# Kernel tuning notes

Hardware: AMD Instinct MI355X
Metric: run time of the kernel (lower is better)

## Reference

```python
import jax, jax.numpy as jnp
import numpy as np
from jax import lax

# Per-tensor power-of-two scales (ScalingImplType.CONST / POWER_OF_TWO in Brevitas)
S_ACT8 = 2.0 ** -4   # 8-bit signed input quant scale
S_ACT4 = 2.0 ** -1   # 4-bit signed input quant scale
S_W = 2.0 ** -2      # per-tensor weight quant scale
S_RELU = 2.0 ** -2   # 4-bit unsigned QuantReLU scale


def fq(x, scale, qmin, qmax):
    # fake-quant with straight-through estimator (STE)
    q = jnp.clip(jnp.round(x / scale), qmin, qmax) * scale
    return x + lax.stop_gradient(q - x)


def fq_signed(x, scale, bits):
    return fq(x, scale, -(2 ** (bits - 1)), 2 ** (bits - 1) - 1)


def fq_uint(x, scale, bits):
    return fq(x, scale, 0, 2 ** bits - 1)


def qconv(x, w, in_bits, w_bits, s_in, stride=1, padding=0, groups=1):
    xq = fq_signed(x, s_in, in_bits)
    wq = fq_signed(w, S_W, w_bits)
    return lax.conv_general_dilated(
        xq, wq, (stride, stride), [(padding, padding)] * 2,
        feature_group_count=groups,
        dimension_numbers=('NCHW', 'OIHW', 'NCHW'))


def maxpool(x, k, s):
    return lax.reduce_window(x, -jnp.inf, lax.max,
                             (1, 1, k, k), (1, 1, s, s), 'VALID')


def dwsep(x, dw, pw):
    c = x.shape[1]
    x = qconv(x, dw, 4, 4, S_ACT4, padding=1, groups=c)  # depthwise 3x3
    x = qconv(x, pw, 4, 4, S_ACT4)                       # pointwise 1x1
    return x


def qrelu4(x):
    return fq_uint(jax.nn.relu(x), S_RELU, 4)


def setup_inputs() -> dict:
    key = jax.random.key(0)
    ks = jax.random.split(key, 10)
    B = 1024
    mk = lambda k, shp, sc=0.5: jax.random.normal(k, shp, jnp.float32) * sc
    return {
        'x': jax.random.normal(ks[0], (B, 3, 32, 32), jnp.float32),
        'w0': mk(ks[1], (3, 3, 1, 1)),
        'dw1': mk(ks[2], (3, 1, 3, 3)),
        'pw1': mk(ks[3], (32, 3, 1, 1)),
        'dw2': mk(ks[4], (32, 1, 3, 3)),
        'pw2': mk(ks[5], (64, 32, 1, 1)),
        'dw3': mk(ks[6], (64, 1, 3, 3)),
        'pw3': mk(ks[7], (128, 64, 1, 1)),
        'wc1': mk(ks[8], (256, 128, 1, 1)),
        'wc2': mk(ks[9], (10, 256, 1, 1)),
    }


def reference(x, w0, dw1, pw1, dw2, pw2, dw3, pw3, wc1, wc2):
    # features
    h = qconv(x, w0, 8, 8, S_ACT8)            # 1x1, 3->3, 8-bit
    h = dwsep(h, dw1, pw1)                    # 3->32, 32x32
    h = qrelu4(h)
    h = maxpool(h, 2, 2)                      # 16x16
    h = dwsep(h, dw2, pw2)                    # 32->64
    h = qrelu4(h)
    h = maxpool(h, 2, 2)                      # 8x8
    h = dwsep(h, dw3, pw3)                    # 64->128
    h = qrelu4(h)
    h = maxpool(h, 8, 1)                      # 1x1
    # classifier
    h = qconv(h, wc1, 4, 4, S_ACT4)           # 128->256
    h = qrelu4(h)
    h = qconv(h, wc2, 4, 4, S_ACT4)           # 256->10
    h = fq_signed(h, S_ACT8, 8)               # output quant int8
    return h
```

## Files before the change

kernel.cpp:

```cpp
#include <hip/hip_runtime.h>

typedef int v4i __attribute__((ext_vector_type(4)));

#define W0i   0
#define DW1i  9
#define PW1i  36
#define DW2i  132
#define WC1p  3556
#define WC2p  11748
#define PW2Fb 12388
#define PW3Fb 12900
#define DW2pk 14948
#define DW3pk 15092
#define WTOT  15380

__device__ __attribute__((aligned(16))) int g_wsq[WTOT];

__device__ __forceinline__ int iclamp(int v, int lo, int hi) {
  return v < lo ? lo : (v > hi ? hi : v);
}
__device__ __forceinline__ int rne4(int a) {
  return (a + 1 + ((a >> 2) & 1)) >> 2;
}
__device__ __forceinline__ int rne32(int a) {
  return (a + 15 + ((a >> 5) & 1)) >> 5;
}

__device__ __forceinline__ void bar_lds() {
  asm volatile("s_waitcnt lgkmcnt(0)\n\ts_barrier" ::: "memory");
}

__device__ __forceinline__ int dot4(int a, int b, int c) {
#if defined(__has_builtin) && __has_builtin(__builtin_amdgcn_sdot4)
  return __builtin_amdgcn_sdot4(a, b, c, false);
#else
  c += ((a << 24) >> 24) * ((b << 24) >> 24);
  c += ((a << 16) >> 24) * ((b << 16) >> 24);
  c += ((a <<  8) >> 24) * ((b <<  8) >> 24);
  c += (a >> 24) * (b >> 24);
  return c;
#endif
}

__device__ __forceinline__ int alignb(int hi, int lo, int sh) {
#if defined(__has_builtin) && __has_builtin(__builtin_amdgcn_alignbyte)
  return __builtin_amdgcn_alignbyte(hi, lo, sh);
#else
  return (int)(((((unsigned long long)(unsigned)hi) << 32) |
                (unsigned)lo) >> (8 * sh));
#endif
}

__device__ __forceinline__ int pack3(int a, int b, int c) {
  return (a & 0xff) | ((b & 0xff) << 8) | ((c & 0xff) << 16);
}

__device__ __forceinline__ int pk_mad16(int a, int b, int c) {
  int d;
  asm("v_pk_mad_i16 %0, %1, %2, %3" : "=v"(d) : "v"(a), "v"(b), "v"(c));
  return d;
}
__device__ __forceinline__ int pk_add16(int a, int b) {
  int d;
  asm("v_pk_add_i16 %0, %1, %2" : "=v"(d) : "v"(a), "v"(b));
  return d;
}
__device__ __forceinline__ int pk_ashr16(int sh, int a) {
  int d;
  asm("v_pk_ashrrev_i16 %0, %1, %2" : "=v"(d) : "v"(sh), "v"(a));
  return d;
}
__device__ __forceinline__ int pk_max16(int a, int b) {
  int d;
  asm("v_pk_max_i16 %0, %1, %2" : "=v"(d) : "v"(a), "v"(b));
  return d;
}
__device__ __forceinline__ int pk_min16(int a, int b) {
  int d;
  asm("v_pk_min_i16 %0, %1, %2" : "=v"(d) : "v"(a), "v"(b));
  return d;
}
__device__ __forceinline__ int rne4s_pk(int a) {
  const int sh = 0x00020002, one = 0x00010001;
  int t = pk_ashr16(sh, a);
  t &= one;
  t += one;
  int s4 = pk_add16(a, t);
  int r = pk_ashr16(sh, s4);
  r = pk_max16(r, (int)0xFFF8FFF8);
  r = pk_min16(r, 0x00070007);
  return r;
}

__device__ __forceinline__ int max4(v4i d) {
  int a = d[0] > d[1] ? d[0] : d[1];
  int b = d[2] > d[3] ? d[2] : d[3];
  return a > b ? a : b;
}

__global__ __launch_bounds__(256) void prep_weights(
    const float* __restrict__ w0,  const float* __restrict__ dw1,
    const float* __restrict__ pw1, const float* __restrict__ dw2,
    const float* __restrict__ pw2, const float* __restrict__ dw3,
    const float* __restrict__ pw3, const float* __restrict__ wc1,
    const float* __restrict__ wc2) {
  int t = blockIdx.x * blockDim.x + threadIdx.x;
  if (t >= WTOT) return;
  if (t >= DW2i && t < WC1p) return;
  if (t < DW2i) {
    float w; int lo = -8, hi = 7;
    if (t < DW1i)      { w = w0[t];        lo = -128; hi = 127; }
    else if (t < PW1i)   w = dw1[t - DW1i];
    else                 w = pw1[t - PW1i];
    g_wsq[t] = iclamp((int)rintf(w * 4.f), lo, hi);
  } else if (t < PW2Fb) {
    const float* src = (t < WC2p) ? wc1 + (t - WC1p) * 4
                                  : wc2 + (t - WC2p) * 4;
    int p = 0;
#pragma unroll
    for (int b = 0; b < 4; b++) {
      int c = iclamp((int)rintf(src[b] * 4.f), -8, 7);
      p |= (c & 0xff) << (8 * b);
    }
    g_wsq[t] = p;
  } else if (t < DW2pk) {
    int i = t - PW2Fb;
    int nt = i >> 7, r = i & 127, lane = r >> 1, dw = r & 1;
    int n = nt * 16 + (lane & 15);
    int kb = (lane >> 4) * 8 + dw * 4;
    int p = 0;
#pragma unroll
    for (int b = 0; b < 4; b++) {
      int c = iclamp((int)rintf(pw2[n * 32 + kb + b] * 4.f), -8, 7);
      p |= (c & 0xff) << (8 * b);
    }
    g_wsq[t] = p;
  } else if (t < DW2pk + 144) {
    int i = t - DW2pk;
    int cq = i / 18, r = i - cq * 18, t9 = r >> 1, par = r & 1;
    int wl = iclamp((int)rintf(dw2[(cq * 4 + par) * 9 + t9] * 4.f), -8, 7);
    int wh = iclamp((int)rintf(dw2[(cq * 4 + 2 + par) * 9 + t9] * 4.f), -8, 7);
    g_wsq[t] = (wl & 0xFFFF) | (wh << 16);
  } else {
    int i = t - DW3pk;
    int cq = i / 18, r = i - cq * 18, t9 = r >> 1, par = r & 1;
    int wl = iclamp((int)rintf(dw3[(cq * 4 + par) * 9 + t9] * 4.f), -8, 7);
    int wh = iclamp((int)rintf(dw3[(cq * 4 + 2 + par) * 9 + t9] * 4.f), -8, 7);
    g_wsq[t] = (wl & 0xFFFF) | (wh << 16);
  }
}

__global__ __launch_bounds__(256) void prep_weights_pw3(
    const float* __restrict__ pw3) {
  int t = PW3Fb + blockIdx.x * blockDim.x + threadIdx.x;
  if (t >= DW2pk) return;
  int i = t - PW3Fb;
  int g = i >> 7, r = i & 127, lane = r >> 1, dw = r & 1;
  int nt = g >> 1, kh = g & 1;
  int n = nt * 16 + (lane & 15);
  int kb = kh * 32 + (lane >> 4) * 8 + dw * 4;
  int p = 0;
#pragma unroll
  for (int b = 0; b < 4; b++) {
    int c = iclamp((int)rintf(pw3[n * 64 + kb + b] * 4.f), -8, 7);
    p |= (c & 0xff) << (8 * b);
  }
  g_wsq[t] = p;
}

__global__ __launch_bounds__(256, 4) void fused_net(
    const float* __restrict__ x,
    float* __restrict__ out)
{
  const int img = blockIdx.x;
  const int tid = threadIdx.x;
  const int wv = tid >> 6, lane = tid & 63;
  const int lm = lane & 15, kg = lane >> 4;
  const int* __restrict__ wq = g_wsq;

  __shared__ __align__(16) int bufAi[2560];
  __shared__ __align__(16) int bufBi[2592];

  const int ntp = (wv & 1) * 2;
  const long bw0 = *(const long*)(wq + PW2Fb + (ntp * 64 + lane) * 2);
  const long bw1 = *(const long*)(wq + PW2Fb + ((ntp + 1) * 64 + lane) * 2);
  long b0v[2], b1v[2];
#pragma unroll
  for (int h = 0; h < 2; h++) {
    int nt = wv * 2 + h;
    b0v[h] = *(const long*)(wq + PW3Fb + (nt * 2 + 0) * 128 + lane * 2);
    b1v[h] = *(const long*)(wq + PW3Fb + (nt * 2 + 1) * 128 + lane * 2);
  }

  {
    const float* xim = x + (size_t)img * 3072;
    const int p4 = tid * 4;
    float4 v0 = *(const float4*)(xim + p4);
    float4 v1 = *(const float4*)(xim + 1024 + p4);
    float4 v2 = *(const float4*)(xim + 2048 + p4);
    int w[9];
#pragma unroll
    for (int i = 0; i < 9; i++) w[i] = wq[W0i + i];
#define Q8(v) iclamp((int)rintf((v) * 16.f), -128, 127)
    int a0[4] = {Q8(v0.x), Q8(v0.y), Q8(v0.z), Q8(v0.w)};
    int a1[4] = {Q8(v1.x), Q8(v1.y), Q8(v1.z), Q8(v1.w)};
    int a2[4] = {Q8(v2.x), Q8(v2.y), Q8(v2.z), Q8(v2.w)};
#undef Q8
#pragma unroll
    for (int o = 0; o < 3; o++) {
      int pk = 0;
#pragma unroll
      for (int j = 0; j < 4; j++) {
        int s = a0[j] * w[o * 3] + a1[j] * w[o * 3 + 1] + a2[j] * w[o * 3 + 2];
        pk |= (iclamp(rne32(s), -8, 7) & 0xff) << (8 * j);
      }
      bufAi[o * 256 + tid] = pk;
    }
  }
  bar_lds();

  {
    const int py = tid >> 4, px = tid & 15;
    int wr[3][3], wrh[3][3];
#pragma unroll
    for (int c = 0; c < 3; c++)
#pragma unroll
      for (int ky = 0; ky < 3; ky++) {
        int w = pack3(wq[DW1i + c * 9 + ky * 3],
                      wq[DW1i + c * 9 + ky * 3 + 1],
                      wq[DW1i + c * 9 + ky * 3 + 2]);
        wr[c][ky] = w;
        wrh[c][ky] = w << 8;
      }
    const int s = (px & 1) ? 1 : 3;
    const int D0 = (2 * px - 1) >> 2;
    int V[3][4];
#pragma unroll
    for (int r = 0; r < 4; r++) {
      int rr = 2 * py - 1 + r;
      bool ok = (unsigned)rr < 32u;
#pragma unroll
      for (int c = 0; c < 3; c++) {
        int lo = 0, hi = 0;
        if (ok) {
          const int* ap = bufAi + c * 256 + rr * 8;
          if (px > 0)  lo = ap[D0];
          if (px < 15) hi = ap[D0 + 1];
        }
        V[c][r] = alignb(hi, lo, s);
      }
    }
    int a[4];
#pragma unroll
    for (int dy = 0; dy < 2; dy++) {
      int r01[3];
#pragma unroll
      for (int c = 0; c < 3; c++) {
        int acc0 = 0, acc1 = 0;
#pragma unroll
        for (int ky = 0; ky < 3; ky++) {
          acc0 = dot4(V[c][dy + ky], wr[c][ky], acc0);
          acc1 = dot4(V[c][dy + ky], wrh[c][ky], acc1);
        }
        int p = (int)__builtin_amdgcn_perm((unsigned)acc1, (unsigned)acc0,
                                           0x05040100u);
        r01[c] = rne4s_pk(p);
      }
      unsigned t0 = __builtin_amdgcn_perm((unsigned)r01[1], (unsigned)r01[0],
                                          0x0C0C0400u);
      a[2 * dy] = (int)__builtin_amdgcn_perm((unsigned)r01[2], t0, 0x0C040100u);
      unsigned t1 = __builtin_amdgcn_perm((unsigned)r01[1], (unsigned)r01[0],
                                          0x0C0C0602u);
      a[2 * dy + 1] =
          (int)__builtin_amdgcn_perm((unsigned)r01[2], t1, 0x0C060100u);
    }
#pragma unroll
    for (int it = 0; it < 8; it++) {
      int pk = 0;
#pragma unroll
      for (int j = 0; j < 4; j++) {
        int o = it * 4 + j;
        int wpk = pack3(wq[PW1i + o * 3], wq[PW1i + o * 3 + 1],
                        wq[PW1i + o * 3 + 2]);
        int m0 = dot4(a[0], wpk, 0), m1 = dot4(a[1], wpk, 0);
        int m2 = dot4(a[2], wpk, 0), m3 = dot4(a[3], wpk, 0);
        int mx = max(max(m0, m1), max(m2, m3));
        pk |= iclamp(rne4(mx), 0, 7) << (8 * j);
      }
      bufBi[py * 149 + px * 9 + it] = pk;
    }
  }
  bar_lds();

  {
    const int cq = tid >> 5;
    const int rem = tid & 31;
    const int y = rem >> 1, xh = rem & 1, x0 = xh * 8;
    int we[9], wo[9];
    {
      const int2* wp = (const int2*)(wq + DW2pk + cq * 18);
#pragma unroll
      for (int t9 = 0; t9 < 9; t9++) { int2 v = wp[t9]; we[t9] = v.x; wo[t9] = v.y; }
    }
    int acce[8] = {}, acco[8] = {};
#pragma unroll
    for (int ky = 0; ky < 3; ky++) {
      int yy = y + ky - 1;
      if (yy < 0 || yy > 15) continue;
      int rb = yy * 149 + cq;
      int rd[10];
      rd[0] = (x0 > 0) ? bufBi[rb + (x0 - 1) * 9] : 0;
#pragma unroll
      for (int k = 1; k < 9; k++) rd[k] = bufBi[rb + (x0 - 1 + k) * 9];
      rd[9] = (x0 < 8) ? bufBi[rb + (x0 + 8) * 9] : 0;
      int ee[10], eo[10];
#pragma unroll
      for (int k = 0; k < 10; k++) {
        ee[k] = rd[k] & 0x000F000F;
        eo[k] = (rd[k] >> 8) & 0x000F000F;
      }
#pragma unroll
      for (int j = 0; j < 8; j++)
#pragma unroll
        for (int kx = 0; kx < 3; kx++) {
          acce[j] = pk_mad16(ee[j + kx], we[ky * 3 + kx], acce[j]);
          acco[j] = pk_mad16(eo[j + kx], wo[ky * 3 + kx], acco[j]);
        }
    }
    const int py = y >> 1, dy = y & 1;
#pragma unroll
    for (int j = 0; j < 8; j++) {
      int xx = x0 + j;
      int qp = py * 8 + (xx >> 1);
      int q = qp ^ (py & 3);
      int m = q * 4 + dy * 2 + (xx & 1);
      int re = rne4s_pk(acce[j]);
      int ro = rne4s_pk(acco[j]);
      bufAi[m * 10 + cq] = (re & 0x00FF00FF) | ((ro & 0x00FF00FF) << 8);
    }
  }
  bar_lds();

  {
    const int mtb = (wv >> 1) * 8;
    const signed char* Ab = (const signed char*)bufAi;
    signed char* A2c = (signed char*)bufBi;
    const int n0 = ntp * 16 + lm, n1 = (ntp + 1) * 16 + lm;
#pragma unroll 4
    for (int mt = mtb; mt < mtb + 8; mt++) {
      int m = mt * 16 + lm;
      long av = *(const long*)(Ab + m * 40 + kg * 8);
      v4i d0 = __builtin_amdgcn_mfma_i32_16x16x32_i8(av, bw0, (v4i){0, 0, 0, 0},
                                                     0, 0, 0);
      v4i d1 = __builtin_amdgcn_mfma_i32_16x16x32_i8(av, bw1, (v4i){0, 0, 0, 0},
                                                     0, 0, 0);
      int q = mt * 4 + kg;
      int qp = q ^ ((q >> 3) & 3);
      int py = qp >> 3, px = qp & 7;
      int bb = (py * 137 + px * 17) * 4;
      A2c[bb + n0] = (signed char)iclamp(rne4(max4(d0)), 0, 7);
      A2c[bb + n1] = (signed char)iclamp(rne4(max4(d1)), 0, 7);
    }
  }
  bar_lds();

  {
    int cq2 = tid >> 4;
    int s = tid & 15;
    int y = s >> 1, x0 = (s & 1) << 2;
    int we[9], wo[9];
    {
      const int2* wp = (const int2*)(wq + DW3pk + cq2 * 18);
#pragma unroll
      for (int t9 = 0; t9 < 9; t9++) { int2 v = wp[t9]; we[t9] = v.x; wo[t9] = v.y; }
    }
    int acce[4] = {}, acco[4] = {};
#pragma unroll
    for (int ky = 0; ky < 3; ky++) {
      int yy = y + ky - 1;
      if (yy < 0 || yy > 7) continue;
      int rb = yy * 137 + cq2;
      int rd[6];
      rd[0] = (x0 == 4) ? bufBi[rb + (x0 - 1) * 17] : 0;
      rd[1] = bufBi[rb + x0 * 17];
      rd[2] = bufBi[rb + (x0 + 1) * 17];
      rd[3] = bufBi[rb + (x0 + 2) * 17];
      rd[4] = bufBi[rb + (x0 + 3) * 17];
      rd[5] = (x0 == 0) ? bufBi[rb + (x0 + 4) * 17] : 0;
      int ee[6], eo[6];
#pragma unroll
      for (int k = 0; k < 6; k++) {
        ee[k] = rd[k] & 0x000F000F;
        eo[k] = (rd[k] >> 8) & 0x000F000F;
      }
#pragma unroll
      for (int j = 0; j < 4; j++)
#pragma unroll
        for (int kx = 0; kx < 3; kx++) {
          acce[j] = pk_mad16(ee[j + kx], we[ky * 3 + kx], acce[j]);
          acco[j] = pk_mad16(eo[j + kx], wo[ky * 3 + kx], acco[j]);
        }
    }
#pragma unroll
    for (int j = 0; j < 4; j++) {
      int re = rne4s_pk(acce[j]);
      int ro = rne4s_pk(acco[j]);
      bufAi[(y * 8 + x0 + j) * 18 + cq2] =
          (re & 0x00FF00FF) | ((ro & 0x00FF00FF) << 8);
    }
  }
  int4 wfc[8];
  {
    const int4* wp = (const int4*)(wq + WC1p + tid * 32);
#pragma unroll
    for (int rI = 0; rI < 8; rI++) wfc[rI] = wp[rI];
  }
  bar_lds();

  {
    const signed char* Ab = (const signed char*)bufAi;
    signed char* fcin = (signed char*)bufBi;
    int mx[2] = {-1000000, -1000000};
#pragma unroll
    for (int mt = 0; mt < 4; mt++) {
      int m = mt * 16 + lm;
      long a0 = *(const long*)(Ab + m * 72 + kg * 8);
      long a1 = *(const long*)(Ab + m * 72 + 32 + kg * 8);
#pragma unroll
      for (int h = 0; h < 2; h++) {
        v4i d = __builtin_amdgcn_mfma_i32_16x16x32_i8(a0, b0v[h],
                                                      (v4i){0, 0, 0, 0}, 0, 0, 0);
        d = __builtin_amdgcn_mfma_i32_16x16x32_i8(a1, b1v[h], d, 0, 0, 0);
        int t4 = max4(d);
        mx[h] = mx[h] > t4 ? mx[h] : t4;
      }
    }
#pragma unroll
    for (int h = 0; h < 2; h++) {
      int red = max(mx[h], __shfl_xor(mx[h], 16));
      red = max(red, __shfl_xor(red, 32));
      if (lane < 16)
        fcin[(wv * 2 + h) * 16 + lm] = (signed char)iclamp(rne4(red), 0, 7);
    }
  }
  bar_lds();

  {
    const int4* mp = (const int4*)bufBi;
    int acc = 0;
#pragma unroll
    for (int rI = 0; rI < 8; rI++) {
      int4 a = mp[rI]; int4 w = wfc[rI];
      acc = dot4(a.x, w.x, acc); acc = dot4(a.y, w.y, acc);
      acc = dot4(a.z, w.z, acc); acc = dot4(a.w, w.w, acc);
    }
    ((signed char*)bufAi)[tid] = (signed char)iclamp(rne4(acc), 0, 7);
  }
  bar_lds();

  if (tid < 40) {
    int k = tid >> 2, j = tid & 3;
    const int4* wp = (const int4*)(wq + WC2p + k * 64 + j * 16);
    const int4* ap = (const int4*)bufAi;
    int acc = 0;
#pragma unroll
    for (int r = 0; r < 4; r++) {
      int4 a = ap[j * 4 + r]; int4 w = wp[r];
      acc = dot4(a.x, w.x, acc); acc = dot4(a.y, w.y, acc);
      acc = dot4(a.z, w.z, acc); acc = dot4(a.w, w.w, acc);
    }
    acc += __shfl_xor(acc, 1);
    acc += __shfl_xor(acc, 2);
    if (j == 0) {
      int code = iclamp(2 * acc, -128, 127);
      out[(size_t)img * 10 + k] = (float)code * 0.0625f;
    }
  }
}

extern "C" void kernel_launch(void* const* d_in, const int* in_sizes, int n_in,
                              void* d_out, int out_size, void* d_ws, size_t ws_size,
                              hipStream_t stream) {
  (void)d_ws; (void)ws_size; (void)in_sizes; (void)n_in; (void)out_size;
  const float* x   = (const float*)d_in[0];
  const float* w0  = (const float*)d_in[1];
  const float* dw1 = (const float*)d_in[2];
  const float* pw1 = (const float*)d_in[3];
  const float* dw2 = (const float*)d_in[4];
  const float* pw2 = (const float*)d_in[5];
  const float* dw3 = (const float*)d_in[6];
  const float* pw3 = (const float*)d_in[7];
  const float* wc1 = (const float*)d_in[8];
  const float* wc2 = (const float*)d_in[9];
  float* out = (float*)d_out;

  prep_weights<<<(WTOT + 255) / 256, 256, 0, stream>>>(
      w0, dw1, pw1, dw2, pw2, dw3, pw3, wc1, wc2);
  prep_weights_pw3<<<(DW2pk - PW3Fb + 255) / 256, 256, 0, stream>>>(pw3);
  fused_net<<<1024, 256, 0, stream>>>(x, out);
}
```

Before: 98.83 us.

## Fuse stage-2 depthwise into MFMA pointwise, pad halo buffer, merge prep kernels

The stage-2 depthwise 3x3 now computes its results directly in the MFMA A-operand register layout. It feeds the pointwise 1x1 MFMA straight from registers, which removes an LDS write, a barrier and a re-read. The stage-1 output buffer gains a zero halo, written by a few threads, so the depthwise reads need no bounds branches, and later stages swap which LDS buffer they use. The pw1 and dw1 weights are pre-packed, and the separate pw3 prep kernel is merged into the main prep kernel, saving one launch. The cost is a larger shared buffer, which may reduce occupancy, and more registers held for all four pointwise weight tiles.

```diff
diff --git a/kernel.cpp b/kernel.cpp
--- a/kernel.cpp
+++ b/kernel.cpp
@@ -5,7 +5,8 @@
 #define W0i   0
 #define DW1i  9
 #define PW1i  36
-#define DW2i  132
+#define PW1pk 132
+#define DW1pk 164
 #define WC1p  3556
 #define WC2p  11748
 #define PW2Fb 12388
@@ -54,6 +55,9 @@
 __device__ __forceinline__ int pack3(int a, int b, int c) {
   return (a & 0xff) | ((b & 0xff) << 8) | ((c & 0xff) << 16);
 }
+__device__ __forceinline__ int q4w(float w) {
+  return iclamp((int)rintf(w * 4.f), -8, 7);
+}
 
 __device__ __forceinline__ int pk_mad16(int a, int b, int c) {
   int d;
@@ -106,13 +110,20 @@
     const float* __restrict__ wc2) {
   int t = blockIdx.x * blockDim.x + threadIdx.x;
   if (t >= WTOT) return;
-  if (t >= DW2i && t < WC1p) return;
-  if (t < DW2i) {
+  if (t < 132) {
     float w; int lo = -8, hi = 7;
     if (t < DW1i)      { w = w0[t];        lo = -128; hi = 127; }
     else if (t < PW1i)   w = dw1[t - DW1i];
     else                 w = pw1[t - PW1i];
     g_wsq[t] = iclamp((int)rintf(w * 4.f), lo, hi);
+  } else if (t < PW1pk + 32) {
+    int o = t - PW1pk;
+    g_wsq[t] = pack3(q4w(pw1[3 * o]), q4w(pw1[3 * o + 1]), q4w(pw1[3 * o + 2]));
+  } else if (t < DW1pk + 9) {
+    int i = t - DW1pk;
+    g_wsq[t] = pack3(q4w(dw1[3 * i]), q4w(dw1[3 * i + 1]), q4w(dw1[3 * i + 2]));
+  } else if (t < WC1p) {
+    return;
   } else if (t < PW2Fb) {
     const float* src = (t < WC2p) ? wc1 + (t - WC1p) * 4
                                   : wc2 + (t - WC2p) * 4;
@@ -123,7 +134,7 @@
       p |= (c & 0xff) << (8 * b);
     }
     g_wsq[t] = p;
-  } else if (t < DW2pk) {
+  } else if (t < PW3Fb) {
     int i = t - PW2Fb;
     int nt = i >> 7, r = i & 127, lane = r >> 1, dw = r & 1;
     int n = nt * 16 + (lane & 15);
@@ -135,37 +146,32 @@
       p |= (c & 0xff) << (8 * b);
     }
     g_wsq[t] = p;
-  } else if (t < DW2pk + 144) {
+  } else if (t < DW2pk) {
+    int i = t - PW3Fb;
+    int g = i >> 7, r = i & 127, lane = r >> 1, dw = r & 1;
+    int nt = g >> 1, kh = g & 1;
+    int n = nt * 16 + (lane & 15);
+    int kb = kh * 32 + (lane >> 4) * 8 + dw * 4;
+    int p = 0;
+#pragma unroll
+    for (int b = 0; b < 4; b++) {
+      int c = iclamp((int)rintf(pw3[n * 64 + kb + b] * 4.f), -8, 7);
+      p |= (c & 0xff) << (8 * b);
+    }
+    g_wsq[t] = p;
+  } else if (t < DW3pk) {
     int i = t - DW2pk;
     int cq = i / 18, r = i - cq * 18, t9 = r >> 1, par = r & 1;
-    int wl = iclamp((int)rintf(dw2[(cq * 4 + par) * 9 + t9] * 4.f), -8, 7);
-    int wh = iclamp((int)rintf(dw2[(cq * 4 + 2 + par) * 9 + t9] * 4.f), -8, 7);
+    int wl = q4w(dw2[(cq * 4 + par) * 9 + t9]);
+    int wh = q4w(dw2[(cq * 4 + 2 + par) * 9 + t9]);
     g_wsq[t] = (wl & 0xFFFF) | (wh << 16);
   } else {
     int i = t - DW3pk;
     int cq = i / 18, r = i - cq * 18, t9 = r >> 1, par = r & 1;
-    int wl = iclamp((int)rintf(dw3[(cq * 4 + par) * 9 + t9] * 4.f), -8, 7);
-    int wh = iclamp((int)rintf(dw3[(cq * 4 + 2 + par) * 9 + t9] * 4.f), -8, 7);
+    int wl = q4w(dw3[(cq * 4 + par) * 9 + t9]);
+    int wh = q4w(dw3[(cq * 4 + 2 + par) * 9 + t9]);
     g_wsq[t] = (wl & 0xFFFF) | (wh << 16);
   }
-}
-
-__global__ __launch_bounds__(256) void prep_weights_pw3(
-    const float* __restrict__ pw3) {
-  int t = PW3Fb + blockIdx.x * blockDim.x + threadIdx.x;
-  if (t >= DW2pk) return;
-  int i = t - PW3Fb;
-  int g = i >> 7, r = i & 127, lane = r >> 1, dw = r & 1;
-  int nt = g >> 1, kh = g & 1;
-  int n = nt * 16 + (lane & 15);
-  int kb = kh * 32 + (lane >> 4) * 8 + dw * 4;
-  int p = 0;
-#pragma unroll
-  for (int b = 0; b < 4; b++) {
-    int c = iclamp((int)rintf(pw3[n * 64 + kb + b] * 4.f), -8, 7);
-    p |= (c & 0xff) << (8 * b);
-  }
-  g_wsq[t] = p;
 }
 
 __global__ __launch_bounds__(256, 4) void fused_net(
@@ -179,11 +185,12 @@
   const int* __restrict__ wq = g_wsq;
 
   __shared__ __align__(16) int bufAi[2560];
-  __shared__ __align__(16) int bufBi[2592];
-
-  const int ntp = (wv & 1) * 2;
-  const long bw0 = *(const long*)(wq + PW2Fb + (ntp * 64 + lane) * 2);
-  const long bw1 = *(const long*)(wq + PW2Fb + ((ntp + 1) * 64 + lane) * 2);
+  __shared__ __align__(16) int bufBi[3240];
+
+  long bwv[4];
+#pragma unroll
+  for (int nt = 0; nt < 4; nt++)
+    bwv[nt] = *(const long*)(wq + PW2Fb + (nt * 64 + lane) * 2);
   long b0v[2], b1v[2];
 #pragma unroll
   for (int h = 0; h < 2; h++) {
@@ -220,15 +227,24 @@
   bar_lds();
 
   {
+    if (tid < 68) {
+      int ry, cx;
+      if (tid < 18)      { ry = 0;        cx = tid; }
+      else if (tid < 36) { ry = 17;       cx = tid - 18; }
+      else if (tid < 52) { ry = tid - 35; cx = 0; }
+      else               { ry = tid - 51; cx = 17; }
+      int base = ry * 180 + cx * 10;
+#pragma unroll
+      for (int h = 0; h < 4; h++)
+        *(long*)(bufBi + base + 2 * h) = 0;
+    }
     const int py = tid >> 4, px = tid & 15;
     int wr[3][3], wrh[3][3];
 #pragma unroll
     for (int c = 0; c < 3; c++)
 #pragma unroll
       for (int ky = 0; ky < 3; ky++) {
-        int w = pack3(wq[DW1i + c * 9 + ky * 3],
-                      wq[DW1i + c * 9 + ky * 3 + 1],
-                      wq[DW1i + c * 9 + ky * 3 + 2]);
+        int w = wq[DW1pk + c * 3 + ky];
         wr[c][ky] = w;
         wrh[c][ky] = w << 8;
       }
@@ -274,92 +290,75 @@
       a[2 * dy + 1] =
           (int)__builtin_amdgcn_perm((unsigned)r01[2], t1, 0x0C060100u);
     }
+    const int wb = (py + 1) * 180 + (px + 1) * 10;
 #pragma unroll
     for (int it = 0; it < 8; it++) {
       int pk = 0;
 #pragma unroll
       for (int j = 0; j < 4; j++) {
-        int o = it * 4 + j;
-        int wpk = pack3(wq[PW1i + o * 3], wq[PW1i + o * 3 + 1],
-                        wq[PW1i + o * 3 + 2]);
+        int wpk = wq[PW1pk + it * 4 + j];
         int m0 = dot4(a[0], wpk, 0), m1 = dot4(a[1], wpk, 0);
         int m2 = dot4(a[2], wpk, 0), m3 = dot4(a[3], wpk, 0);
         int mx = max(max(m0, m1), max(m2, m3));
         pk |= iclamp(rne4(mx), 0, 7) << (8 * j);
       }
-      bufBi[py * 149 + px * 9 + it] = pk;
-    }
-  }
-  bar_lds();
-
-  {
-    const int cq = tid >> 5;
-    const int rem = tid & 31;
-    const int y = rem >> 1, xh = rem & 1, x0 = xh * 8;
-    int we[9], wo[9];
+      bufBi[wb + it] = pk;
+    }
+  }
+  bar_lds();
+
+  {
+    int we0[9], wo0[9], we1[9], wo1[9];
     {
-      const int2* wp = (const int2*)(wq + DW2pk + cq * 18);
-#pragma unroll
-      for (int t9 = 0; t9 < 9; t9++) { int2 v = wp[t9]; we[t9] = v.x; wo[t9] = v.y; }
-    }
-    int acce[8] = {}, acco[8] = {};
-#pragma unroll
-    for (int ky = 0; ky < 3; ky++) {
-      int yy = y + ky - 1;
-      if (yy < 0 || yy > 15) continue;
-      int rb = yy * 149 + cq;
-      int rd[10];
-      rd[0] = (x0 > 0) ? bufBi[rb + (x0 - 1) * 9] : 0;
-#pragma unroll
-      for (int k = 1; k < 9; k++) rd[k] = bufBi[rb + (x0 - 1 + k) * 9];
-      rd[9] = (x0 < 8) ? bufBi[rb + (x0 + 8) * 9] : 0;
-      int ee[10], eo[10];
-#pragma unroll
-      for (int k = 0; k < 10; k++) {
-        ee[k] = rd[k] & 0x000F000F;
-        eo[k] = (rd[k] >> 8) & 0x000F000F;
-      }
-#pragma unroll
-      for (int j = 0; j < 8; j++)
+      const int2* wp0 = (const int2*)(wq + DW2pk + (2 * kg) * 18);
+      const int2* wp1 = (const int2*)(wq + DW2pk + (2 * kg + 1) * 18);
+#pragma unroll
+      for (int t9 = 0; t9 < 9; t9++) {
+        int2 v0 = wp0[t9]; we0[t9] = v0.x; wo0[t9] = v0.y;
+        int2 v1 = wp1[t9]; we1[t9] = v1.x; wo1[t9] = v1.y;
+      }
+    }
+    long av[4];
+#pragma unroll
+    for (int mi = 0; mi < 4; mi++) {
+      int m = (wv * 4 + mi) * 16 + lm;
+      int q = m >> 2, d = m & 3;
+      int qp = q ^ ((q >> 3) & 3);
+      int y = 2 * (qp >> 3) + (d >> 1);
+      int xx = 2 * (qp & 7) + (d & 1);
+      int acce0 = 0, acco0 = 0, acce1 = 0, acco1 = 0;
+#pragma unroll
+      for (int ky = 0; ky < 3; ky++) {
+        const int rb = (y + ky) * 180 + xx * 10 + 2 * kg;
 #pragma unroll
         for (int kx = 0; kx < 3; kx++) {
-          acce[j] = pk_mad16(ee[j + kx], we[ky * 3 + kx], acce[j]);
-          acco[j] = pk_mad16(eo[j + kx], wo[ky * 3 + kx], acco[j]);
+          long rv = *(const long*)(bufBi + rb + kx * 10);
+          int d0 = (int)rv, d1 = (int)(((unsigned long long)rv) >> 32);
+          int wi = ky * 3 + kx;
+          acce0 = pk_mad16(d0 & 0x000F000F, we0[wi], acce0);
+          acco0 = pk_mad16((d0 >> 8) & 0x000F000F, wo0[wi], acco0);
+          acce1 = pk_mad16(d1 & 0x000F000F, we1[wi], acce1);
+          acco1 = pk_mad16((d1 >> 8) & 0x000F000F, wo1[wi], acco1);
         }
-    }
-    const int py = y >> 1, dy = y & 1;
-#pragma unroll
-    for (int j = 0; j < 8; j++) {
-      int xx = x0 + j;
-      int qp = py * 8 + (xx >> 1);
-      int q = qp ^ (py & 3);
-      int m = q * 4 + dy * 2 + (xx & 1);
-      int re = rne4s_pk(acce[j]);
-      int ro = rne4s_pk(acco[j]);
-      bufAi[m * 10 + cq] = (re & 0x00FF00FF) | ((ro & 0x00FF00FF) << 8);
-    }
-  }
-  bar_lds();
-
-  {
-    const int mtb = (wv >> 1) * 8;
-    const signed char* Ab = (const signed char*)bufAi;
-    signed char* A2c = (signed char*)bufBi;
-    const int n0 = ntp * 16 + lm, n1 = (ntp + 1) * 16 + lm;
-#pragma unroll 4
-    for (int mt = mtb; mt < mtb + 8; mt++) {
-      int m = mt * 16 + lm;
-      long av = *(const long*)(Ab + m * 40 + kg * 8);
-      v4i d0 = __builtin_amdgcn_mfma_i32_16x16x32_i8(av, bw0, (v4i){0, 0, 0, 0},
-                                                     0, 0, 0);
-      v4i d1 = __builtin_amdgcn_mfma_i32_16x16x32_i8(av, bw1, (v4i){0, 0, 0, 0},
-                                                     0, 0, 0);
-      int q = mt * 4 + kg;
-      int qp = q ^ ((q >> 3) & 3);
-      int py = qp >> 3, px = qp & 7;
-      int bb = (py * 137 + px * 17) * 4;
-      A2c[bb + n0] = (signed char)iclamp(rne4(max4(d0)), 0, 7);
-      A2c[bb + n1] = (signed char)iclamp(rne4(max4(d1)), 0, 7);
+      }
+      int re0 = rne4s_pk(acce0), ro0 = rne4s_pk(acco0);
+      int re1 = rne4s_pk(acce1), ro1 = rne4s_pk(acco1);
+      unsigned lo32 = (unsigned)((re0 & 0x00FF00FF) | ((ro0 & 0x00FF00FF) << 8));
+      unsigned hi32 = (unsigned)((re1 & 0x00FF00FF) | ((ro1 & 0x00FF00FF) << 8));
+      av[mi] = (long)(((unsigned long long)hi32 << 32) | lo32);
+    }
+    signed char* A2c = (signed char*)bufAi;
+#pragma unroll
+    for (int mi = 0; mi < 4; mi++) {
+      int q2 = (wv * 4 + mi) * 4 + kg;
+      int qp2 = q2 ^ ((q2 >> 3) & 3);
+      int bb = ((qp2 >> 3) * 137 + (qp2 & 7) * 17) * 4;
+#pragma unroll
+      for (int nt = 0; nt < 4; nt++) {
+        v4i d = __builtin_amdgcn_mfma_i32_16x16x32_i8(av[mi], bwv[nt],
+                                                      (v4i){0, 0, 0, 0}, 0, 0, 0);
+        A2c[bb + nt * 16 + lm] = (signed char)iclamp(rne4(max4(d)), 0, 7);
+      }
     }
   }
   bar_lds();
@@ -381,12 +380,12 @@
       if (yy < 0 || yy > 7) continue;
       int rb = yy * 137 + cq2;
       int rd[6];
-      rd[0] = (x0 == 4) ? bufBi[rb + (x0 - 1) * 17] : 0;
-      rd[1] = bufBi[rb + x0 * 17];
-      rd[2] = bufBi[rb + (x0 + 1) * 17];
-      rd[3] = bufBi[rb + (x0 + 2) * 17];
-      rd[4] = bufBi[rb + (x0 + 3) * 17];
-      rd[5] = (x0 == 0) ? bufBi[rb + (x0 + 4) * 17] : 0;
+      rd[0] = (x0 == 4) ? bufAi[rb + (x0 - 1) * 17] : 0;
+      rd[1] = bufAi[rb + x0 * 17];
+      rd[2] = bufAi[rb + (x0 + 1) * 17];
+      rd[3] = bufAi[rb + (x0 + 2) * 17];
+      rd[4] = bufAi[rb + (x0 + 3) * 17];
+      rd[5] = (x0 == 0) ? bufAi[rb + (x0 + 4) * 17] : 0;
       int ee[6], eo[6];
 #pragma unroll
       for (int k = 0; k < 6; k++) {
@@ -405,7 +404,7 @@
     for (int j = 0; j < 4; j++) {
       int re = rne4s_pk(acce[j]);
       int ro = rne4s_pk(acco[j]);
-      bufAi[(y * 8 + x0 + j) * 18 + cq2] =
+      bufBi[(y * 8 + x0 + j) * 18 + cq2] =
           (re & 0x00FF00FF) | ((ro & 0x00FF00FF) << 8);
     }
   }
@@ -418,8 +417,8 @@
   bar_lds();
 
   {
-    const signed char* Ab = (const signed char*)bufAi;
-    signed char* fcin = (signed char*)bufBi;
+    const signed char* Ab = (const signed char*)bufBi;
+    signed char* fcin = (signed char*)bufAi;
     int mx[2] = {-1000000, -1000000};
 #pragma unroll
     for (int mt = 0; mt < 4; mt++) {
@@ -446,7 +445,7 @@
   bar_lds();
 
   {
-    const int4* mp = (const int4*)bufBi;
+    const int4* mp = (const int4*)bufAi;
     int acc = 0;
 #pragma unroll
     for (int rI = 0; rI < 8; rI++) {
@@ -454,14 +453,14 @@
       acc = dot4(a.x, w.x, acc); acc = dot4(a.y, w.y, acc);
       acc = dot4(a.z, w.z, acc); acc = dot4(a.w, w.w, acc);
     }
-    ((signed char*)bufAi)[tid] = (signed char)iclamp(rne4(acc), 0, 7);
+    ((signed char*)bufBi)[tid] = (signed char)iclamp(rne4(acc), 0, 7);
   }
   bar_lds();
 
   if (tid < 40) {
     int k = tid >> 2, j = tid & 3;
     const int4* wp = (const int4*)(wq + WC2p + k * 64 + j * 16);
-    const int4* ap = (const int4*)bufAi;
+    const int4* ap = (const int4*)bufBi;
     int acc = 0;
 #pragma unroll
     for (int r = 0; r < 4; r++) {
@@ -496,6 +495,5 @@
 
   prep_weights<<<(WTOT + 255) / 256, 256, 0, stream>>>(
       w0, dw1, pw1, dw2, pw2, dw3, pw3, wc1, wc2);
-  prep_weights_pw3<<<(DW2pk - PW3Fb + 255) / 256, 256, 0, stream>>>(pw3);
   fused_net<<<1024, 256, 0, stream>>>(x, out);
 }
```

Measured after the change: 93.59 us. 1.06x faster.
